# Kernel optimization log

Measured on AMD Instinct MI355X. Metric: run time of the kernel, lower is better.

The kernel has to match this reference:

```python
import jax, jax.numpy as jnp
import numpy as np

H = 16
D_MODEL = 1024
D_K = D_MODEL // H


def setup_inputs() -> dict:
    key = jax.random.key(0)
    ks = jax.random.split(key, 8)
    B, S = 4, 2048
    query = jax.random.normal(ks[0], (B, S, D_MODEL), dtype=jnp.float32)
    key_t = jax.random.normal(ks[1], (B, S, D_MODEL), dtype=jnp.float32)
    value = jax.random.normal(ks[2], (B, S, D_MODEL), dtype=jnp.float32)
    mask = jax.random.randint(ks[3], (B, S, S), 0, 2, dtype=jnp.int32)
    sc = 1.0 / np.sqrt(D_MODEL)
    Wq = jax.random.normal(ks[4], (D_MODEL, D_MODEL), dtype=jnp.float32) * sc
    Wk = jax.random.normal(ks[5], (D_MODEL, D_MODEL), dtype=jnp.float32) * sc
    Wv = jax.random.normal(ks[6], (D_MODEL, D_MODEL), dtype=jnp.float32) * sc
    Wo = jax.random.normal(ks[7], (D_MODEL, D_MODEL), dtype=jnp.float32) * sc
    return {"query": query, "key": key_t, "value": value, "mask": mask,
            "Wq": Wq, "Wk": Wk, "Wv": Wv, "Wo": Wo}


def reference(query, key, value, mask, Wq, Wk, Wv, Wo):
    B, S, _ = query.shape
    # nn.Linear(bias=False): y = x @ W^T; then split heads -> [B,H,S,d_k]
    def proj(x, W):
        return (x @ W.T).reshape(B, S, H, D_K).transpose(0, 2, 1, 3)

    q = proj(query, Wq)
    k = proj(key, Wk)
    v = proj(value, Wv)

    m = (mask[:, None, :, :] != 0)  # [B,1,S,S] broadcast over heads
    scores = jnp.einsum('bhqd,bhkd->bhqk', q, k) / jnp.sqrt(jnp.float32(D_K))
    scores = jnp.where(m, scores, jnp.float32(-1e9))
    p_attn = jax.nn.softmax(scores, axis=-1)
    p_attn = jnp.where(m, p_attn, 0.0)
    # dropout is identity in eval mode
    x = jnp.einsum('bhqk,bhkd->bhqd', p_attn, v)
    x = x.transpose(0, 2, 1, 3).reshape(B, S, D_MODEL)
    return x @ Wo.T
```

## Files before the change

kernel.cpp:

```cpp
#include <hip/hip_runtime.h>


typedef __attribute__((ext_vector_type(8))) short frag8;
typedef __attribute__((ext_vector_type(4))) float f32x4;
typedef unsigned long long ull;

#define MFMA16(a,b,c) __builtin_amdgcn_mfma_f32_16x16x32_bf16((a),(b),(c),0,0,0)

__device__ __forceinline__ short f2bf(float f) {
  union { float f; unsigned u; } x; x.f = f;
  unsigned r = (x.u + 0x7fffu + ((x.u >> 16) & 1u)) >> 16;
  return (short)r;
}

__device__ __forceinline__ unsigned pkbf(float lo, float hi) {
  union { float f; unsigned u; } a, b;
  a.f = lo; b.f = hi;
  return __builtin_amdgcn_perm(b.u + 0x8000u, a.u + 0x8000u, 0x07060302u);
}

__device__ __forceinline__ unsigned pkbf_t(float lo, float hi) {
  union { float f; unsigned u; } a, b;
  a.f = lo; b.f = hi;
  return __builtin_amdgcn_perm(b.u, a.u, 0x07060302u);
}

__device__ __forceinline__ unsigned bit2m(unsigned word, int off) {
  unsigned r;
  asm("v_bfe_i32 %0, %1, %2, 1" : "=v"(r) : "v"(word), "v"(off));
  return r;
}
__device__ __forceinline__ unsigned mk2(unsigned word, int base) {
  return __builtin_amdgcn_perm(bit2m(word, base + 1), bit2m(word, base),
                               0x05040100u);
}

__device__ __forceinline__ void gl16(const void* g, void* l) {
  __builtin_amdgcn_global_load_lds(
      (const __attribute__((address_space(1))) unsigned*)g,
      (__attribute__((address_space(3))) unsigned*)l, 16, 0, 0);
}

__global__ __launch_bounds__(256) void prep(
    const float* __restrict__ q, const float* __restrict__ k,
    const float* __restrict__ v, const int* __restrict__ msk,
    const float* __restrict__ wq, const float* __restrict__ wk,
    const float* __restrict__ wv, const float* __restrict__ wo,
    short* __restrict__ qo, short* __restrict__ ko, short* __restrict__ vo,
    short* __restrict__ oq, short* __restrict__ ok, short* __restrict__ ov,
    short* __restrict__ oo, ull* __restrict__ bits) {
  int bid = blockIdx.x;
  if (bid < 24576) {
    int z = bid >> 13;
    int i = (bid & 8191) * 256 + threadIdx.x;
    const float* s = z == 0 ? q : z == 1 ? k : v;
    short* d = z == 0 ? qo : z == 1 ? ko : vo;
    float4 f = ((const float4*)s)[i];
    short4 o;
    o.x = f2bf(f.x); o.y = f2bf(f.y); o.z = f2bf(f.z); o.w = f2bf(f.w);
    ((short4*)d)[i] = o;
  } else if (bid < 28672) {
    int zb = bid - 24576;
    int z = zb >> 10;
    int i = (zb & 1023) * 256 + threadIdx.x;
    const float* s = z == 0 ? wq : z == 1 ? wk : z == 2 ? wv : wo;
    short* d = z == 0 ? oq : z == 1 ? ok : z == 2 ? ov : oo;
    float sc = (z == 0) ? 0.18033688011f : 1.0f;
    float4 f = ((const float4*)s)[i];
    short4 o;
    o.x = f2bf(f.x * sc); o.y = f2bf(f.y * sc);
    o.z = f2bf(f.z * sc); o.w = f2bf(f.w * sc);
    ((short4*)d)[i] = o;
  } else {
    int zb = bid - 28672;
    int wv_ = threadIdx.x >> 6, l = threadIdx.x & 63;
    size_t row = (size_t)zb * 4 + wv_;
    const int* src = msk + row * 2048;
    for (int c = 0; c < 2048; c += 64) {
      ull bl = __ballot(src[c + l] != 0);
      if (l == 0) bits[(size_t)(c >> 6) * 8192 + row] = bl;
    }
  }
}

template <int MODE>
__device__ __forceinline__ void gemm_body(const short* __restrict__ A,
                                          const short* __restrict__ W,
                                          void* __restrict__ outp, int bid) {
  __shared__ short As[2][128 * 32];
  __shared__ short Bs[2][128 * 32];
  const int t = threadIdx.x;
  const int l = t & 63, wv = t >> 6;
  const int lg = l >> 4, lr = l & 15;
  const int wm = (wv >> 1) * 64, wn = (wv & 1) * 64;
  const int m0 = (bid >> 3) * 128;
  const int n0 = (bid & 7) * 128;

  auto stage = [&](int buf, int kt) {
    const int k0 = kt * 32;
#pragma unroll
    for (int c = 0; c < 2; ++c) {
      int idx = c * 256 + t;
      int row = idx >> 2, ch = (idx & 3) * 8;
      gl16(A + (size_t)(m0 + row) * 1024 + k0 + ch, &As[buf][idx * 8]);
      gl16(W + (size_t)(n0 + row) * 1024 + k0 + ch, &Bs[buf][idx * 8]);
    }
  };

  f32x4 acc[4][4] = {};
  stage(0, 0);
  asm volatile("s_waitcnt vmcnt(0)" ::: "memory");
  __syncthreads();
  int buf = 0;
  for (int kt = 0; kt < 32; ++kt) {
    if (kt + 1 < 32) stage(buf ^ 1, kt + 1);
    frag8 af[4], bf[4];
#pragma unroll
    for (int i = 0; i < 4; ++i) {
      af[i] = *(const frag8*)&As[buf][(wm + i * 16 + lr) * 32 + 8 * lg];
      bf[i] = *(const frag8*)&Bs[buf][(wn + i * 16 + lr) * 32 + 8 * lg];
    }
    __builtin_amdgcn_s_setprio(1);
#pragma unroll
    for (int mi = 0; mi < 4; ++mi)
#pragma unroll
      for (int ni = 0; ni < 4; ++ni)
        acc[mi][ni] = MFMA16(af[mi], bf[ni], acc[mi][ni]);
    __builtin_amdgcn_s_setprio(0);
    asm volatile("s_waitcnt vmcnt(0)" ::: "memory");
    __syncthreads();
    buf ^= 1;
  }

#pragma unroll
  for (int mi = 0; mi < 4; ++mi)
#pragma unroll
    for (int ni = 0; ni < 4; ++ni)
#pragma unroll
      for (int r = 0; r < 4; ++r) {
        int m = m0 + wm + mi * 16 + 4 * lg + r;
        int n = n0 + wn + ni * 16 + lr;
        if (MODE == 0) {
          int b = m >> 11, s = m & 2047, h = n >> 6, dk = n & 63;
          ((short*)outp)[(((size_t)b * 16 + h) * 2048 + s) * 64 + dk] =
              f2bf(acc[mi][ni][r]);
        } else {
          ((float*)outp)[(size_t)m * 1024 + n] = acc[mi][ni][r];
        }
      }
}

__global__ __launch_bounds__(256) void gemm_qkv(
    const short* __restrict__ A0, const short* __restrict__ A1,
    const short* __restrict__ A2, const short* __restrict__ W0,
    const short* __restrict__ W1, const short* __restrict__ W2,
    short* __restrict__ O0, short* __restrict__ O1, short* __restrict__ O2) {
  int wg = (blockIdx.x & 7) * 192 + (blockIdx.x >> 3);
  int z = wg >> 9, bid = wg & 511;
  const short* A = z == 0 ? A0 : z == 1 ? A1 : A2;
  const short* W = z == 0 ? W0 : z == 1 ? W1 : W2;
  short* O = z == 0 ? O0 : z == 1 ? O1 : O2;
  gemm_body<0>(A, W, O, bid);
}

__global__ __launch_bounds__(256) void gemm_o(
    const short* __restrict__ A, const short* __restrict__ W,
    float* __restrict__ O) {
  int bid = (blockIdx.x & 7) * 64 + (blockIdx.x >> 3);
  gemm_body<1>(A, W, O, bid);
}

__global__ __launch_bounds__(256) void transpose_v(
    const short* __restrict__ Vp, short* __restrict__ Vt) {
  __shared__ short lds[64 * 72];
  int bh = blockIdx.y, s0 = blockIdx.x * 64;
  int t = threadIdx.x;
  int rr = t >> 3, c0 = (t & 7) * 8;
#pragma unroll
  for (int half = 0; half < 2; ++half) {
    int r = half * 32 + rr;
    frag8 v = *(const frag8*)(Vp + ((size_t)bh * 2048 + s0 + r) * 64 + c0);
#pragma unroll
    for (int j = 0; j < 8; ++j) lds[r * 72 + c0 + j] = v[j];
  }
  __syncthreads();
#pragma unroll
  for (int half = 0; half < 2; ++half) {
    int d = half * 32 + rr;
    frag8 o;
#pragma unroll
    for (int j = 0; j < 8; ++j) o[j] = lds[(c0 + j) * 72 + d];
    *(frag8*)(Vt + ((size_t)bh * 64 + d) * 2048 + s0 + c0) = o;
  }
}

__global__ __launch_bounds__(512, 4) void attn_fwd(
    const short* __restrict__ Qp, const short* __restrict__ Kp,
    const short* __restrict__ Vt, const ull* __restrict__ mb64,
    short* __restrict__ X) {
  __shared__ __align__(16) short smem[20480];

  const int wg = (blockIdx.x & 7) * 128 + (blockIdx.x >> 3);
  const int qt = wg & 15, bh = wg >> 4;
  const int b = bh >> 4, h = bh & 15;
  const int t = threadIdx.x;
  const int l = t & 63, wv = t >> 6;
  const int lg = l >> 4, lr = l & 15;
  const int pw = wv >> 1, kvh = wv & 1;
  const int q0 = qt * 128 + pw * 32;
  const int qrow_base = b << 11;

  frag8 qf[2][2];
  const short* Qb = Qp + ((size_t)bh * 2048 + q0) * 64;
#pragma unroll
  for (int qb = 0; qb < 2; ++qb)
#pragma unroll
    for (int kc = 0; kc < 2; ++kc)
      qf[qb][kc] = *(const frag8*)(Qb + (qb * 16 + lr) * 64 + kc * 32 + 8 * lg);

  f32x4 acc[4][2] = {};
  f32x4 accl[2] = {};

  const size_t kbase = (size_t)bh * 2048 * 64;
  const size_t vbase = (size_t)bh * 64 * 2048;
  short* Pw = &smem[16384 + wv * 512];
  const int sx = lr & 7;
  const int sxp = (lr >> 1) & 3;

  frag8 ones;
#pragma unroll
  for (int j = 0; j < 8; ++j) ones[j] = (short)0x3F80;

  const int srow = t >> 3, sc = t & 7;
  const int scs = (sc ^ (srow & 7)) * 8;
  auto stageK = [&](int buf, int kt) {
    gl16(Kp + kbase + (size_t)(kt * 64 + srow) * 64 + scs,
         &smem[buf * 4096 + t * 8]);
  };
  auto stageV = [&](int buf, int kt) {
    gl16(Vt + vbase + (size_t)srow * 2048 + kt * 64 + scs,
         &smem[8192 + buf * 4096 + t * 8]);
  };

  const unsigned* mbp32 = (const unsigned*)mb64;
  const int row0 = qrow_base + q0 + lr;
  const int row1 = row0 + 16;
  unsigned mw0 = mbp32[(size_t)row0 * 2 + kvh];
  unsigned mw1 = mbp32[(size_t)row1 * 2 + kvh];

  stageK(0, 0);
  stageV(0, 0);
  asm volatile("s_waitcnt vmcnt(0)" ::: "memory");
  __syncthreads();
  int buf = 0;

  for (int kt = 0; kt < 32; ++kt) {
    unsigned mwc0 = mw0, mwc1 = mw1;
    const int nk = (kt + 1) & 31;
    mw0 = mbp32[((size_t)nk * 8192 + row0) * 2 + kvh];
    mw1 = mbp32[((size_t)nk * 8192 + row1) * 2 + kvh];
    stageV(buf ^ 1, nk);
    stageK(buf ^ 1, nk);

    const short* Kb = &smem[buf * 4096];
    f32x4 s[2][2] = {};
    __builtin_amdgcn_s_setprio(1);
#pragma unroll
    for (int nb = 0; nb < 2; ++nb) {
      const int ro = (kvh * 32 + nb * 16 + lr) * 64;
      frag8 k0 = *(const frag8*)&Kb[ro + ((0 + lg) ^ sx) * 8];
      frag8 k1 = *(const frag8*)&Kb[ro + ((4 + lg) ^ sx) * 8];
#pragma unroll
      for (int qb = 0; qb < 2; ++qb) {
        s[nb][qb] = MFMA16(k0, qf[qb][0], s[nb][qb]);
        s[nb][qb] = MFMA16(k1, qf[qb][1], s[nb][qb]);
      }
    }
    __builtin_amdgcn_s_setprio(0);

    auto softmax_store = [&](int qb, unsigned word) {
      const int q32 = lr * 32;
#pragma unroll
      for (int nb = 0; nb < 2; ++nb) {
        int base = nb * 16 + 4 * lg;
        float e0 = __builtin_amdgcn_exp2f(s[nb][qb][0]);
        float e1 = __builtin_amdgcn_exp2f(s[nb][qb][1]);
        float e2 = __builtin_amdgcn_exp2f(s[nb][qb][2]);
        float e3 = __builtin_amdgcn_exp2f(s[nb][qb][3]);
        uint2 w;
        w.x = pkbf_t(e0, e1) & mk2(word, base);
        w.y = pkbf_t(e2, e3) & mk2(word, base + 2);
        int sw = ((2 * nb + (lg >> 1)) ^ sxp) * 8 + 4 * (lg & 1);
        *(uint2*)&Pw[q32 + sw] = w;
      }
    };

    frag8 pf0, pf1;
    softmax_store(0, mwc0);
    pf0 = *(const frag8*)&Pw[lr * 32 + ((lg ^ sxp)) * 8];
    softmax_store(1, mwc1);
    pf1 = *(const frag8*)&Pw[lr * 32 + ((lg ^ sxp)) * 8];

    const short* Vb = &smem[8192 + buf * 4096];
    __builtin_amdgcn_s_setprio(1);
#pragma unroll
    for (int db = 0; db < 4; ++db) {
      frag8 vf = *(const frag8*)&Vb[(db * 16 + lr) * 64 +
                                    ((kvh * 4 + lg) ^ sx) * 8];
      acc[db][0] = MFMA16(vf, pf0, acc[db][0]);
      acc[db][1] = MFMA16(vf, pf1, acc[db][1]);
    }
    accl[0] = MFMA16(ones, pf0, accl[0]);
    accl[1] = MFMA16(ones, pf1, accl[1]);
    __builtin_amdgcn_s_setprio(0);

    asm volatile("s_waitcnt vmcnt(0)" ::: "memory");
    __syncthreads();
    buf ^= 1;
  }

  float* mf = (float*)smem;
  __syncthreads();
  if (kvh) {
#pragma unroll
    for (int i = 0; i < 8; ++i)
      *(f32x4*)&mf[pw * 2048 + i * 256 + l * 4] = acc[i >> 1][i & 1];
#pragma unroll
    for (int qb = 0; qb < 2; ++qb)
      *(f32x4*)&mf[8192 + pw * 512 + qb * 256 + l * 4] = accl[qb];
  }
  __syncthreads();
  if (!kvh) {
#pragma unroll
    for (int i = 0; i < 8; ++i) {
      f32x4 p = *(const f32x4*)&mf[pw * 2048 + i * 256 + l * 4];
      acc[i >> 1][i & 1] += p;
    }
#pragma unroll
    for (int qb = 0; qb < 2; ++qb) {
      f32x4 p = *(const f32x4*)&mf[8192 + pw * 512 + qb * 256 + l * 4];
      accl[qb] += p;
    }
#pragma unroll
    for (int qb = 0; qb < 2; ++qb) {
      float inv = 1.0f / fmaxf(accl[qb][0], 1e-30f);
      int q = q0 + qb * 16 + lr;
      size_t base = (size_t)(qrow_base + q) * 1024 + h * 64 + 4 * lg;
#pragma unroll
      for (int db = 0; db < 4; ++db) {
        uint2 o;
        o.x = pkbf(acc[db][qb][0] * inv, acc[db][qb][1] * inv);
        o.y = pkbf(acc[db][qb][2] * inv, acc[db][qb][3] * inv);
        *(uint2*)&X[base + db * 16] = o;
      }
    }
  }
}

extern "C" void kernel_launch(void* const* d_in, const int* in_sizes, int n_in,
                              void* d_out, int out_size, void* d_ws,
                              size_t ws_size, hipStream_t stream) {
  const float* q  = (const float*)d_in[0];
  const float* k  = (const float*)d_in[1];
  const float* v  = (const float*)d_in[2];
  const int*  msk = (const int*)d_in[3];
  const float* Wq = (const float*)d_in[4];
  const float* Wk = (const float*)d_in[5];
  const float* Wv = (const float*)d_in[6];
  const float* Wo = (const float*)d_in[7];

  const size_t SZ_T = 16777216;
  const size_t SZ_W = 2097152;
  char* ws = (char*)d_ws;
  short* qb  = (short*)(ws + 0 * SZ_T);
  short* kb  = (short*)(ws + 1 * SZ_T);
  short* vb  = (short*)(ws + 2 * SZ_T);
  short* Qp  = (short*)(ws + 3 * SZ_T);
  short* Kp  = (short*)(ws + 4 * SZ_T);
  short* Vp  = (short*)(ws + 5 * SZ_T);
  short* Vt  = (short*)(ws + 6 * SZ_T);
  short* X   = (short*)(ws + 7 * SZ_T);
  short* wqb = (short*)(ws + 8 * SZ_T);
  short* wkb = (short*)(ws + 8 * SZ_T + 1 * SZ_W);
  short* wvb = (short*)(ws + 8 * SZ_T + 2 * SZ_W);
  short* wob = (short*)(ws + 8 * SZ_T + 3 * SZ_W);
  void*  mb  = (void*)(ws + 8 * SZ_T + 4 * SZ_W);
  if (ws_size < 8 * SZ_T + 5 * SZ_W) return;

  prep<<<30720, 256, 0, stream>>>(q, k, v, msk, Wq, Wk, Wv, Wo,
                                  qb, kb, vb, wqb, wkb, wvb, wob, (ull*)mb);
  gemm_qkv<<<1536, 256, 0, stream>>>(qb, kb, vb, wqb, wkb, wvb, Qp, Kp, Vp);
  transpose_v<<<dim3(32, 64), 256, 0, stream>>>(Vp, Vt);
  attn_fwd<<<1024, 512, 0, stream>>>(Qp, Kp, Vt, (const ull*)mb, X);
  gemm_o<<<512, 256, 0, stream>>>(X, wob, (float*)d_out);
}
```

Baseline: 254.5 us.

## Keep softmax P in registers by permuting V transpose key order

The transposed V layout is permuted so the key order inside each 8-element chunk matches the MFMA output register layout of the score tiles. The P fragments for the PV MFMA can then be assembled directly in registers instead of round-tripping through LDS, which removes the per-iteration P scratch region and its stores and loads. Shared memory shrinks from 40KB to 32KB, which may improve occupancy. The epilogue reduction is split into two phases so the row-sum buffer fits in the smaller LDS.

```diff
diff --git a/kernel.cpp b/kernel.cpp
--- a/kernel.cpp
+++ b/kernel.cpp
@@ -184,12 +184,16 @@
     for (int j = 0; j < 8; ++j) lds[r * 72 + c0 + j] = v[j];
   }
   __syncthreads();
+  const int hh = c0 >> 5, g = (c0 & 31) >> 3;
 #pragma unroll
   for (int half = 0; half < 2; ++half) {
     int d = half * 32 + rr;
     frag8 o;
 #pragma unroll
-    for (int j = 0; j < 8; ++j) o[j] = lds[(c0 + j) * 72 + d];
+    for (int j = 0; j < 8; ++j) {
+      int sp = hh * 32 + ((j < 4) ? (4 * g + j) : (16 + 4 * g + (j - 4)));
+      o[j] = lds[sp * 72 + d];
+    }
     *(frag8*)(Vt + ((size_t)bh * 64 + d) * 2048 + s0 + c0) = o;
   }
 }
@@ -198,7 +202,7 @@
     const short* __restrict__ Qp, const short* __restrict__ Kp,
     const short* __restrict__ Vt, const ull* __restrict__ mb64,
     short* __restrict__ X) {
-  __shared__ __align__(16) short smem[20480];
+  __shared__ __align__(16) short smem[16384];
 
   const int wg = (blockIdx.x & 7) * 128 + (blockIdx.x >> 3);
   const int qt = wg & 15, bh = wg >> 4;
@@ -223,9 +227,7 @@
 
   const size_t kbase = (size_t)bh * 2048 * 64;
   const size_t vbase = (size_t)bh * 64 * 2048;
-  short* Pw = &smem[16384 + wv * 512];
   const int sx = lr & 7;
-  const int sxp = (lr >> 1) & 3;
 
   frag8 ones;
 #pragma unroll
@@ -278,28 +280,30 @@
     }
     __builtin_amdgcn_s_setprio(0);
 
-    auto softmax_store = [&](int qb, unsigned word) {
-      const int q32 = lr * 32;
-#pragma unroll
-      for (int nb = 0; nb < 2; ++nb) {
-        int base = nb * 16 + 4 * lg;
-        float e0 = __builtin_amdgcn_exp2f(s[nb][qb][0]);
-        float e1 = __builtin_amdgcn_exp2f(s[nb][qb][1]);
-        float e2 = __builtin_amdgcn_exp2f(s[nb][qb][2]);
-        float e3 = __builtin_amdgcn_exp2f(s[nb][qb][3]);
-        uint2 w;
-        w.x = pkbf_t(e0, e1) & mk2(word, base);
-        w.y = pkbf_t(e2, e3) & mk2(word, base + 2);
-        int sw = ((2 * nb + (lg >> 1)) ^ sxp) * 8 + 4 * (lg & 1);
-        *(uint2*)&Pw[q32 + sw] = w;
+    auto softmax_pf = [&](int qb, unsigned word) -> frag8 {
+      union { uint4 u; frag8 f; } cv;
+      {
+        int base = 4 * lg;
+        float e0 = __builtin_amdgcn_exp2f(s[0][qb][0]);
+        float e1 = __builtin_amdgcn_exp2f(s[0][qb][1]);
+        float e2 = __builtin_amdgcn_exp2f(s[0][qb][2]);
+        float e3 = __builtin_amdgcn_exp2f(s[0][qb][3]);
+        cv.u.x = pkbf_t(e0, e1) & mk2(word, base);
+        cv.u.y = pkbf_t(e2, e3) & mk2(word, base + 2);
       }
+      {
+        int base = 16 + 4 * lg;
+        float e0 = __builtin_amdgcn_exp2f(s[1][qb][0]);
+        float e1 = __builtin_amdgcn_exp2f(s[1][qb][1]);
+        float e2 = __builtin_amdgcn_exp2f(s[1][qb][2]);
+        float e3 = __builtin_amdgcn_exp2f(s[1][qb][3]);
+        cv.u.z = pkbf_t(e0, e1) & mk2(word, base);
+        cv.u.w = pkbf_t(e2, e3) & mk2(word, base + 2);
+      }
+      return cv.f;
     };
-
-    frag8 pf0, pf1;
-    softmax_store(0, mwc0);
-    pf0 = *(const frag8*)&Pw[lr * 32 + ((lg ^ sxp)) * 8];
-    softmax_store(1, mwc1);
-    pf1 = *(const frag8*)&Pw[lr * 32 + ((lg ^ sxp)) * 8];
+    frag8 pf0 = softmax_pf(0, mwc0);
+    frag8 pf1 = softmax_pf(1, mwc1);
 
     const short* Vb = &smem[8192 + buf * 4096];
     __builtin_amdgcn_s_setprio(1);
@@ -323,11 +327,22 @@
   __syncthreads();
   if (kvh) {
 #pragma unroll
+    for (int qb = 0; qb < 2; ++qb)
+      *(f32x4*)&mf[(pw * 2 + qb) * 256 + l * 4] = accl[qb];
+  }
+  __syncthreads();
+  if (!kvh) {
+#pragma unroll
+    for (int qb = 0; qb < 2; ++qb) {
+      f32x4 p = *(const f32x4*)&mf[(pw * 2 + qb) * 256 + l * 4];
+      accl[qb] += p;
+    }
+  }
+  __syncthreads();
+  if (kvh) {
+#pragma unroll
     for (int i = 0; i < 8; ++i)
       *(f32x4*)&mf[pw * 2048 + i * 256 + l * 4] = acc[i >> 1][i & 1];
-#pragma unroll
-    for (int qb = 0; qb < 2; ++qb)
-      *(f32x4*)&mf[8192 + pw * 512 + qb * 256 + l * 4] = accl[qb];
   }
   __syncthreads();
   if (!kvh) {
@@ -335,11 +350,6 @@
     for (int i = 0; i < 8; ++i) {
       f32x4 p = *(const f32x4*)&mf[pw * 2048 + i * 256 + l * 4];
       acc[i >> 1][i & 1] += p;
-    }
-#pragma unroll
-    for (int qb = 0; qb < 2; ++qb) {
-      f32x4 p = *(const f32x4*)&mf[8192 + pw * 512 + qb * 256 + l * 4];
-      accl[qb] += p;
     }
 #pragma unroll
     for (int qb = 0; qb < 2; ++qb) {
```

New measurement: 239.6 us. 5.9% less time.
